# Performance work log

Hardware: AMD Instinct MI355X
Metric: run time of the kernel (lower is better)

The kernel has to match this reference:

```python
import jax, jax.numpy as jnp
import numpy as np

N_NODES = 50000
NUM_LAYERS = 3
D = 128
NUM_LABELS = 16
NUM_EDGES = 1600000


def setup_inputs() -> dict:
    key = jax.random.key(0)
    ks = jax.random.split(key, 6)
    s = 1.0 / np.sqrt(D)
    x = jax.random.normal(ks[0], (N_NODES, D), dtype=jnp.float32)
    edge_index = jax.random.randint(ks[1], (2, NUM_EDGES), 0, N_NODES, dtype=jnp.int64)
    W1 = jax.random.normal(ks[2], (NUM_LAYERS, D, D), dtype=jnp.float32) * s
    b1 = jnp.zeros((NUM_LAYERS, D), dtype=jnp.float32)
    W2 = jax.random.normal(ks[3], (NUM_LAYERS, D, D), dtype=jnp.float32) * s
    b2 = jnp.zeros((NUM_LAYERS, D), dtype=jnp.float32)
    Wc = jax.random.normal(ks[4], (D, NUM_LABELS), dtype=jnp.float32) * s
    bc = jnp.zeros((NUM_LABELS,), dtype=jnp.float32)
    return {"x": x, "edge_index": edge_index, "W1": W1, "b1": b1,
            "W2": W2, "b2": b2, "Wc": Wc, "bc": bc}


def reference(x, edge_index, W1, b1, W2, b2, Wc, bc):
    # PyG GINConv (default eps=0): h_i = MLP((1+eps)*x_i + sum_{j->i} x_j)
    src, dst = edge_index[0], edge_index[1]
    h = x
    for l in range(NUM_LAYERS):
        agg = jax.ops.segment_sum(h[src], dst, num_segments=N_NODES)  # [N, D]
        z = h + agg
        h = jax.nn.relu(z @ W1[l] + b1[l]) @ W2[l] + b2[l]
    logits = h @ Wc + bc
    return (h, logits)
```

## Files before the change

### kernel.cpp

```cpp
#include <hip/hip_runtime.h>

#define DD 128
#define CHUNK 6144
#define NBMAX 512
#define SCAP 8192
#define PADSLACK 2048

typedef __attribute__((ext_vector_type(8))) short bf16x8;
typedef __attribute__((ext_vector_type(4))) float f32x4;

__device__ __forceinline__ unsigned bf16rne(float f) {
  unsigned u = __float_as_uint(f);
  return (u + 0x7FFFu + ((u >> 16) & 1u)) >> 16;
}
__device__ __forceinline__ unsigned packbf(float lo, float hi) {
  return bf16rne(lo) | (bf16rne(hi) << 16);
}
__device__ __forceinline__ float bflo(unsigned v) { return __uint_as_float(v << 16); }
__device__ __forceinline__ float bfhi(unsigned v) { return __uint_as_float(v & 0xFFFF0000u); }

__device__ void block_scan_incl(int* cnt, int* inc, int nb, int tid) {
  for (int i = tid; i < nb; i += 256) inc[i] = cnt[i];
  __syncthreads();
  for (int d = 1; d < nb; d <<= 1) {
    int i0 = tid, i1 = tid + 256;
    int v0 = 0, v1 = 0;
    if (i0 < nb && i0 >= d) v0 = inc[i0 - d];
    if (i1 < nb && i1 >= d) v1 = inc[i1 - d];
    __syncthreads();
    if (i0 < nb) inc[i0] += v0;
    if (i1 < nb) inc[i1] += v1;
    __syncthreads();
  }
}

__global__ __launch_bounds__(256) void s1_hist(const int* __restrict__ dst,
                                               int* __restrict__ bucketCount, int e) {
  __shared__ int h[NBMAX];
  int tid = threadIdx.x;
  for (int i = tid; i < NBMAX; i += 256) h[i] = 0;
  __syncthreads();
  int i0 = blockIdx.x * CHUNK;
  int i1 = min(i0 + CHUNK, e);
  for (int i = i0 + tid; i < i1; i += 256) atomicAdd(&h[dst[i] >> 7], 1);
  __syncthreads();
  for (int i = tid; i < NBMAX; i += 256)
    if (h[i]) atomicAdd(&bucketCount[i], h[i]);
}

__global__ __launch_bounds__(256) void s2_scan(const int* __restrict__ bucketCount,
                                               int* __restrict__ bucketOff,
                                               int* __restrict__ gCursor,
                                               int* __restrict__ rs, int nb, int n, int e) {
  __shared__ int cnt[NBMAX], inc[NBMAX];
  int tid = threadIdx.x;
  for (int i = tid; i < nb; i += 256) cnt[i] = bucketCount[i];
  __syncthreads();
  block_scan_incl(cnt, inc, nb, tid);
  for (int i = tid; i < nb; i += 256) {
    int off = inc[i] - cnt[i];
    bucketOff[i] = off;
    gCursor[i] = off;
  }
  if (tid == 0) { bucketOff[nb] = e; rs[n] = e; }
}

__global__ __launch_bounds__(256) void s3_scatter(const int* __restrict__ src,
                                                  const int* __restrict__ dst,
                                                  int* __restrict__ gCursor,
                                                  unsigned int* __restrict__ bucketed,
                                                  int e, int nb) {
  __shared__ int cnt[NBMAX], inc[NBMAX], base[NBMAX], cur[NBMAX];
  __shared__ unsigned int pairs[CHUNK];
  int tid = threadIdx.x;
  for (int i = tid; i < nb; i += 256) cnt[i] = 0;
  __syncthreads();
  int i0 = blockIdx.x * CHUNK;
  int i1 = min(i0 + CHUNK, e);
  for (int i = i0 + tid; i < i1; i += 256) atomicAdd(&cnt[dst[i] >> 7], 1);
  __syncthreads();
  block_scan_incl(cnt, inc, nb, tid);
  for (int b = tid; b < nb; b += 256) {
    int c = cnt[b];
    base[b] = c ? atomicAdd(&gCursor[b], c) : 0;
    cur[b] = inc[b] - c;
  }
  __syncthreads();
  for (int i = i0 + tid; i < i1; i += 256) {
    int d = dst[i];
    int p = atomicAdd(&cur[d >> 7], 1);
    pairs[p] = (unsigned)d | ((unsigned)src[i] << 16);
  }
  __syncthreads();
  int m = i1 - i0;
  for (int i = tid; i < m; i += 256) {
    unsigned w = pairs[i];
    int b = (int)(w & 0xFFFFu) >> 7;
    bucketed[base[b] + (i - (inc[b] - cnt[b]))] = w;
  }
}

__global__ __launch_bounds__(256) void s4_fill(const unsigned int* __restrict__ bucketed,
                                               const int* __restrict__ bucketOff,
                                               int* __restrict__ rs,
                                               unsigned short* __restrict__ pdeg,
                                               unsigned short* __restrict__ ssrc, int n) {
  __shared__ int cnt[128], pin[128], cur[128];
  __shared__ unsigned short outb[SCAP];
  int b = blockIdx.x;
  int bo = bucketOff[b], b1 = bucketOff[b + 1];
  int len = b1 - bo;
  int pstart = bo + b * PADSLACK;
  int tid = threadIdx.x;
  int n0 = b << 7;
  if (tid < 128) cnt[tid] = 0;
  __syncthreads();
  for (int i = tid; i < len; i += 256) atomicAdd(&cnt[bucketed[bo + i] & 127], 1);
  __syncthreads();
  int pc = 0;
  if (tid < 128) {
    pc = max(16, (cnt[tid] + 15) & ~15);
    pin[tid] = pc;
  }
  __syncthreads();
  for (int d = 1; d < 128; d <<= 1) {
    int v = 0;
    if (tid < 128 && tid >= d) v = pin[tid - d];
    __syncthreads();
    if (tid < 128) pin[tid] += v;
    __syncthreads();
  }
  int plen = pin[127];
  if (tid < 128) {
    int off = pin[tid] - pc;
    cur[tid] = off;
    int node = n0 + tid;
    if (node < n) {
      rs[node] = pstart + off;
      pdeg[node] = (unsigned short)pc;
    }
  }
  __syncthreads();
  if (plen <= SCAP) {
    for (int i = tid; i < plen; i += 256) outb[i] = (unsigned short)n;
    __syncthreads();
    for (int i = tid; i < len; i += 256) {
      unsigned w = bucketed[bo + i];
      int p = atomicAdd(&cur[w & 127], 1);
      outb[p] = (unsigned short)(w >> 16);
    }
    __syncthreads();
    for (int i = tid; i < plen; i += 256) ssrc[pstart + i] = outb[i];
  } else {
    for (int i = tid; i < plen; i += 256) ssrc[pstart + i] = (unsigned short)n;
    __syncthreads();
    for (int i = tid; i < len; i += 256) {
      unsigned w = bucketed[bo + i];
      int p = atomicAdd(&cur[w & 127], 1);
      ssrc[pstart + p] = (unsigned short)(w >> 16);
    }
  }
}

__global__ __launch_bounds__(256) void conv_bf16(const float* __restrict__ x,
                                                 unsigned int* __restrict__ hb,
                                                 int n64, int total64) {
  int i = blockIdx.x * 256 + threadIdx.x;
  if (i < n64) {
    float2 v = ((const float2*)x)[i];
    hb[i] = packbf(v.x, v.y);
  } else if (i < total64) {
    hb[i] = 0u;
  }
}

__global__ __launch_bounds__(256) void prep_w(const float* __restrict__ W1,
                                              const float* __restrict__ W2,
                                              short* __restrict__ wt) {
  int idx = blockIdx.x * 256 + threadIdx.x;
  if (idx >= 3 * 2 * 16384) return;
  int lm = idx >> 14;
  int e = idx & 16383;
  int k = e >> 7;
  int col = e & 127;
  int layer = lm >> 1, mat = lm & 1;
  const float* W = mat ? W2 : W1;
  float w = W[layer * 16384 + k * 128 + col];
  unsigned short h = (unsigned short)bf16rne(w);
  int ksw = k ^ ((col & 7) << 3);
  wt[(size_t)lm * 16384 + col * 128 + ksw] = (short)h;
}

__global__ __launch_bounds__(256) void gather_zb(const unsigned int* __restrict__ hb,
                                                 const int* __restrict__ rs,
                                                 const unsigned short* __restrict__ pdeg,
                                                 const unsigned short* __restrict__ ssrc,
                                                 unsigned int* __restrict__ zb, int n) {
  int node = blockIdx.x * 4 + (threadIdx.x >> 6);
  if (node >= n) return;
  int lane = threadIdx.x & 63;
  int s0 = rs[node];
  int m = pdeg[node];
  unsigned v = hb[(unsigned)node * 64u + lane];
  float ax = bflo(v), ay = bfhi(v);
  unsigned A[16], B[16];
#pragma unroll
  for (int i = 0; i < 16; ++i)
    A[i] = hb[(unsigned)ssrc[s0 + i] * 64u + lane];
  int t1 = s0 + m;
  for (int t = s0 + 16; t < t1; t += 16) {
#pragma unroll
    for (int i = 0; i < 16; ++i)
      B[i] = hb[(unsigned)ssrc[t + i] * 64u + lane];
#pragma unroll
    for (int i = 0; i < 16; ++i) {
      ax += bflo(A[i]);
      ay += bfhi(A[i]);
    }
#pragma unroll
    for (int i = 0; i < 16; ++i) A[i] = B[i];
  }
#pragma unroll
  for (int i = 0; i < 16; ++i) {
    ax += bflo(A[i]);
    ay += bfhi(A[i]);
  }
  zb[(unsigned)node * 64u + lane] = packbf(ax, ay);
}

__global__ __launch_bounds__(256, 2) void mlp_mfma(
    const unsigned int* __restrict__ zb,
    const short* __restrict__ Wt1, const short* __restrict__ Wt2,
    const float* __restrict__ b1, const float* __restrict__ b2,
    float* __restrict__ fout, unsigned short* __restrict__ hbout,
    const float* __restrict__ Wc, const float* __restrict__ bc,
    float* __restrict__ lout, int n) {
  __shared__ char wbuf[32768];
  __shared__ char hsb[128 * 256];
  int tid = threadIdx.x;
  int w = tid >> 6, lane = tid & 63;
  int lr = lane & 15, hi = lane >> 4;
  int wr = (w & 1) * 64;
  int wc = (w >> 1) * 64;
  int node0 = blockIdx.x * 128;

  bf16x8 a[4][4];
#pragma unroll
  for (int t = 0; t < 4; ++t) {
    int row = node0 + wr + t * 16 + lr;
    row = min(row, n - 1);
    const char* rp = (const char*)(zb + (size_t)row * 64);
#pragma unroll
    for (int ks = 0; ks < 4; ++ks)
      a[t][ks] = *(const bf16x8*)(rp + ks * 64 + hi * 16);
  }

  f32x4 acc[4][4];
#pragma unroll
  for (int ct = 0; ct < 4; ++ct) {
    float bb = b1[wc + ct * 16 + lr];
#pragma unroll
    for (int t = 0; t < 4; ++t) acc[t][ct] = (f32x4){bb, bb, bb, bb};
  }

  {
    const char* gs = (const char*)Wt1;
    for (int i = tid * 16; i < 32768; i += 256 * 16)
      *(float4*)&wbuf[i] = *(const float4*)(gs + i);
  }
  __syncthreads();
#pragma unroll
  for (int ct = 0; ct < 4; ++ct) {
    int col = wc + ct * 16 + lr;
    int cx = (col & 7) << 4;
#pragma unroll
    for (int ks = 0; ks < 4; ++ks) {
      bf16x8 b = *(const bf16x8*)&wbuf[(col * 256 + ks * 64 + hi * 16) ^ cx];
#pragma unroll
      for (int t = 0; t < 4; ++t)
        acc[t][ct] = __builtin_amdgcn_mfma_f32_16x16x32_bf16(a[t][ks], b, acc[t][ct], 0, 0, 0);
    }
  }

#pragma unroll
  for (int t = 0; t < 4; ++t)
#pragma unroll
    for (int ct = 0; ct < 4; ++ct)
#pragma unroll
      for (int r = 0; r < 4; ++r) {
        int row = wr + t * 16 + hi * 4 + r;
        int col = wc + ct * 16 + lr;
        float v = fmaxf(acc[t][ct][r], 0.f);
        int byte = (row * 256 + col * 2) ^ ((row & 7) << 4);
        *(unsigned short*)&hsb[byte] = (unsigned short)bf16rne(v);
      }
  __syncthreads();

  bf16x8 a2[4][4];
#pragma unroll
  for (int t = 0; t < 4; ++t) {
    int row = wr + t * 16 + lr;
    int xr = (row & 7) << 4;
#pragma unroll
    for (int ks = 0; ks < 4; ++ks)
      a2[t][ks] = *(const bf16x8*)&hsb[(row * 256 + ks * 64 + hi * 16) ^ xr];
  }

#pragma unroll
  for (int ct = 0; ct < 4; ++ct) {
    float bb = b2[wc + ct * 16 + lr];
#pragma unroll
    for (int t = 0; t < 4; ++t) acc[t][ct] = (f32x4){bb, bb, bb, bb};
  }

  __syncthreads();
  {
    const char* gs = (const char*)Wt2;
    for (int i = tid * 16; i < 32768; i += 256 * 16)
      *(float4*)&wbuf[i] = *(const float4*)(gs + i);
  }
  __syncthreads();
#pragma unroll
  for (int ct = 0; ct < 4; ++ct) {
    int col = wc + ct * 16 + lr;
    int cx = (col & 7) << 4;
#pragma unroll
    for (int ks = 0; ks < 4; ++ks) {
      bf16x8 b = *(const bf16x8*)&wbuf[(col * 256 + ks * 64 + hi * 16) ^ cx];
#pragma unroll
      for (int t = 0; t < 4; ++t)
        acc[t][ct] = __builtin_amdgcn_mfma_f32_16x16x32_bf16(a2[t][ks], b, acc[t][ct], 0, 0, 0);
    }
  }

#pragma unroll
  for (int t = 0; t < 4; ++t)
#pragma unroll
    for (int ct = 0; ct < 4; ++ct)
#pragma unroll
      for (int r = 0; r < 4; ++r) {
        int node = node0 + wr + t * 16 + hi * 4 + r;
        if (node < n) {
          int col = wc + ct * 16 + lr;
          float v = acc[t][ct][r];
          if (fout) fout[(size_t)node * DD + col] = v;
          if (hbout) hbout[(size_t)node * DD + col] = (unsigned short)bf16rne(v);
        }
      }

  if (lout) {
    __syncthreads();
    float* wcb = (float*)wbuf;
    for (int i = tid; i < DD * 16; i += 256) wcb[i] = Wc[i];
#pragma unroll
    for (int t = 0; t < 4; ++t)
#pragma unroll
      for (int ct = 0; ct < 4; ++ct)
#pragma unroll
        for (int r = 0; r < 4; ++r) {
          int row = wr + t * 16 + hi * 4 + r;
          int col = wc + ct * 16 + lr;
          int byte = (row * 256 + col * 2) ^ ((row & 7) << 4);
          *(unsigned short*)&hsb[byte] = (unsigned short)bf16rne(acc[t][ct][r]);
        }
    __syncthreads();
    int node = tid >> 1;
    int lbase = (tid & 1) * 8;
    float lacc[8];
#pragma unroll
    for (int j = 0; j < 8; ++j) lacc[j] = bc[lbase + j];
    int xr = (node & 7) << 4;
    for (int c = 0; c < DD; ++c) {
      unsigned short hv16 = *(const unsigned short*)&hsb[(node * 256 + c * 2) ^ xr];
      float hv = __uint_as_float((unsigned)hv16 << 16);
      const float* wrow = &wcb[c * 16 + lbase];
#pragma unroll
      for (int j = 0; j < 8; ++j) lacc[j] += hv * wrow[j];
    }
    int gn = node0 + node;
    if (gn < n) {
#pragma unroll
      for (int j = 0; j < 8; ++j) lout[(size_t)gn * 16 + lbase + j] = lacc[j];
    }
  }
}

extern "C" void kernel_launch(void* const* d_in, const int* in_sizes, int n_in,
                              void* d_out, int out_size, void* d_ws, size_t ws_size,
                              hipStream_t stream) {
  const float* x = (const float*)d_in[0];
  const int* ei = (const int*)d_in[1];
  const float* W1 = (const float*)d_in[2];
  const float* b1 = (const float*)d_in[3];
  const float* W2 = (const float*)d_in[4];
  const float* b2 = (const float*)d_in[5];
  const float* Wc = (const float*)d_in[6];
  const float* bc = (const float*)d_in[7];

  const int N = in_sizes[0] / DD;
  const int E = in_sizes[1] / 2;
  const int* src = ei;
  const int* dst = ei + E;
  const int NB = (N + 127) >> 7;

  float* outp = (float*)d_out;
  float* h_final = outp;
  float* logits = outp + (size_t)N * DD;

  char* ws = (char*)d_ws;
  size_t off = 0;
  auto alloc = [&](size_t bytes) {
    char* p = ws + off;
    off = (off + bytes + 255) & ~(size_t)255;
    return p;
  };
  unsigned int* zb = (unsigned int*)alloc((size_t)N * 64 * 4);
  unsigned int* hb = (unsigned int*)alloc((size_t)(N + 1) * 64 * 4);
  short* wt = (short*)alloc((size_t)3 * 2 * 16384 * 2);
  int* bucketCount = (int*)alloc(NBMAX * 4);
  int* bucketOff = (int*)alloc((NBMAX + 1) * 4);
  int* gCursor = (int*)alloc(NBMAX * 4);
  int* rs = (int*)alloc((size_t)(N + 1) * 4);
  unsigned short* pdeg = (unsigned short*)alloc((size_t)N * 2);
  unsigned int* bucketed = (unsigned int*)alloc((size_t)E * 4);
  unsigned short* ssrc = (unsigned short*)alloc(((size_t)E + (size_t)NB * PADSLACK) * 2);

  const int gEdge = (E + CHUNK - 1) / CHUNK;
  const int gGather = (N + 3) / 4;
  const int gMlp = (N + 127) / 128;
  const int total64 = (N + 1) * 64;

  hipMemsetAsync(bucketCount, 0, NBMAX * 4, stream);
  s1_hist<<<gEdge, 256, 0, stream>>>(dst, bucketCount, E);
  s2_scan<<<1, 256, 0, stream>>>(bucketCount, bucketOff, gCursor, rs, NB, N, E);
  s3_scatter<<<gEdge, 256, 0, stream>>>(src, dst, gCursor, bucketed, E, NB);
  s4_fill<<<NB, 256, 0, stream>>>(bucketed, bucketOff, rs, pdeg, ssrc, N);

  prep_w<<<(3 * 2 * 16384 + 255) / 256, 256, 0, stream>>>(W1, W2, wt);
  conv_bf16<<<(total64 + 255) / 256, 256, 0, stream>>>(x, hb, N * 64, total64);

  auto WT = [&](int layer, int mat) { return wt + ((size_t)(layer * 2 + mat)) * 16384; };

  gather_zb<<<gGather, 256, 0, stream>>>(hb, rs, pdeg, ssrc, zb, N);
  mlp_mfma<<<gMlp, 256, 0, stream>>>(zb, WT(0, 0), WT(0, 1), b1, b2,
                                     nullptr, (unsigned short*)hb, nullptr, nullptr, nullptr, N);
  gather_zb<<<gGather, 256, 0, stream>>>(hb, rs, pdeg, ssrc, zb, N);
  mlp_mfma<<<gMlp, 256, 0, stream>>>(zb, WT(1, 0), WT(1, 1), b1 + DD, b2 + DD,
                                     nullptr, (unsigned short*)hb, nullptr, nullptr, nullptr, N);
  gather_zb<<<gGather, 256, 0, stream>>>(hb, rs, pdeg, ssrc, zb, N);
  mlp_mfma<<<gMlp, 256, 0, stream>>>(zb, WT(2, 0), WT(2, 1), b1 + 2 * DD, b2 + 2 * DD,
                                     h_final, nullptr, Wc, bc, logits, N);
}
```

Baseline: 273.9 us.

## Fuse setup kernels, pad neighbor lists to 8, dual-node gather, MFMA classifier

Merges the histogram, bf16 conversion and weight-prep kernels into one launch, and also preps a swizzled bf16 copy of the classifier weights. Neighbor-list padding drops from multiples of 16 to 8 to cut wasted gather loads, and each wavefront now gathers two nodes with interleaved 8-wide batches to expose more memory parallelism. The mlp kernel prefetches W2 into registers before the first GEMM's epilogue to drop a barrier, and computes logits with MFMA instead of a scalar loop. These changes add register pressure in the gather and mlp kernels and reduce per-node load batching depth.

```diff
diff --git a/kernel.cpp b/kernel.cpp
--- a/kernel.cpp
+++ b/kernel.cpp
@@ -4,7 +4,7 @@
 #define CHUNK 6144
 #define NBMAX 512
 #define SCAP 8192
-#define PADSLACK 2048
+#define PADSLACK 1024
 
 typedef __attribute__((ext_vector_type(8))) short bf16x8;
 typedef __attribute__((ext_vector_type(4))) float f32x4;
@@ -34,18 +34,53 @@
   }
 }
 
-__global__ __launch_bounds__(256) void s1_hist(const int* __restrict__ dst,
-                                               int* __restrict__ bucketCount, int e) {
-  __shared__ int h[NBMAX];
+__global__ __launch_bounds__(256) void setup_fat(
+    const int* __restrict__ dst, int* __restrict__ bucketCount, int e,
+    const float* __restrict__ x, unsigned int* __restrict__ hb, int n64, int total64,
+    const float* __restrict__ W1, const float* __restrict__ W2,
+    const float* __restrict__ Wc, short* __restrict__ wt,
+    int nS1, int nConv) {
+  int b = blockIdx.x;
   int tid = threadIdx.x;
-  for (int i = tid; i < NBMAX; i += 256) h[i] = 0;
-  __syncthreads();
-  int i0 = blockIdx.x * CHUNK;
-  int i1 = min(i0 + CHUNK, e);
-  for (int i = i0 + tid; i < i1; i += 256) atomicAdd(&h[dst[i] >> 7], 1);
-  __syncthreads();
-  for (int i = tid; i < NBMAX; i += 256)
-    if (h[i]) atomicAdd(&bucketCount[i], h[i]);
+  if (b < nS1) {
+    __shared__ int h[NBMAX];
+    for (int i = tid; i < NBMAX; i += 256) h[i] = 0;
+    __syncthreads();
+    int i0 = b * CHUNK;
+    int i1 = min(i0 + CHUNK, e);
+    for (int i = i0 + tid; i < i1; i += 256) atomicAdd(&h[dst[i] >> 7], 1);
+    __syncthreads();
+    for (int i = tid; i < NBMAX; i += 256)
+      if (h[i]) atomicAdd(&bucketCount[i], h[i]);
+  } else if (b < nS1 + nConv) {
+    int i = (b - nS1) * 256 + tid;
+    if (i < n64) {
+      float2 v = ((const float2*)x)[i];
+      hb[i] = packbf(v.x, v.y);
+    } else if (i < total64) {
+      hb[i] = 0u;
+    }
+  } else {
+    int idx = (b - nS1 - nConv) * 256 + tid;
+    if (idx < 3 * 2 * 16384) {
+      int lm = idx >> 14;
+      int e2 = idx & 16383;
+      int k = e2 >> 7;
+      int col = e2 & 127;
+      int layer = lm >> 1, mat = lm & 1;
+      const float* W = mat ? W2 : W1;
+      float w = W[layer * 16384 + k * 128 + col];
+      int ksw = k ^ ((col & 7) << 3);
+      wt[(size_t)lm * 16384 + col * 128 + ksw] = (short)bf16rne(w);
+    } else if (idx < 3 * 2 * 16384 + 2048) {
+      int e2 = idx - 3 * 2 * 16384;
+      int k = e2 >> 4;
+      int col = e2 & 15;
+      float w = Wc[k * 16 + col];
+      int ksw = k ^ ((col & 7) << 3);
+      wt[(size_t)6 * 16384 + col * 128 + ksw] = (short)bf16rne(w);
+    }
+  }
 }
 
 __global__ __launch_bounds__(256) void s2_scan(const int* __restrict__ bucketCount,
@@ -119,7 +154,7 @@
   __syncthreads();
   int pc = 0;
   if (tid < 128) {
-    pc = max(16, (cnt[tid] + 15) & ~15);
+    pc = max(8, (cnt[tid] + 7) & ~7);
     pin[tid] = pc;
   }
   __syncthreads();
@@ -162,70 +197,83 @@
   }
 }
 
-__global__ __launch_bounds__(256) void conv_bf16(const float* __restrict__ x,
-                                                 unsigned int* __restrict__ hb,
-                                                 int n64, int total64) {
-  int i = blockIdx.x * 256 + threadIdx.x;
-  if (i < n64) {
-    float2 v = ((const float2*)x)[i];
-    hb[i] = packbf(v.x, v.y);
-  } else if (i < total64) {
-    hb[i] = 0u;
-  }
-}
-
-__global__ __launch_bounds__(256) void prep_w(const float* __restrict__ W1,
-                                              const float* __restrict__ W2,
-                                              short* __restrict__ wt) {
-  int idx = blockIdx.x * 256 + threadIdx.x;
-  if (idx >= 3 * 2 * 16384) return;
-  int lm = idx >> 14;
-  int e = idx & 16383;
-  int k = e >> 7;
-  int col = e & 127;
-  int layer = lm >> 1, mat = lm & 1;
-  const float* W = mat ? W2 : W1;
-  float w = W[layer * 16384 + k * 128 + col];
-  unsigned short h = (unsigned short)bf16rne(w);
-  int ksw = k ^ ((col & 7) << 3);
-  wt[(size_t)lm * 16384 + col * 128 + ksw] = (short)h;
-}
-
 __global__ __launch_bounds__(256) void gather_zb(const unsigned int* __restrict__ hb,
                                                  const int* __restrict__ rs,
                                                  const unsigned short* __restrict__ pdeg,
                                                  const unsigned short* __restrict__ ssrc,
                                                  unsigned int* __restrict__ zb, int n) {
-  int node = blockIdx.x * 4 + (threadIdx.x >> 6);
-  if (node >= n) return;
+  int pair = blockIdx.x * 4 + (threadIdx.x >> 6);
+  int nA = pair * 2;
+  if (nA >= n) return;
+  int nB = nA + 1;
+  bool hasB = nB < n;
   int lane = threadIdx.x & 63;
-  int s0 = rs[node];
-  int m = pdeg[node];
-  unsigned v = hb[(unsigned)node * 64u + lane];
-  float ax = bflo(v), ay = bfhi(v);
-  unsigned A[16], B[16];
-#pragma unroll
-  for (int i = 0; i < 16; ++i)
-    A[i] = hb[(unsigned)ssrc[s0 + i] * 64u + lane];
-  int t1 = s0 + m;
-  for (int t = s0 + 16; t < t1; t += 16) {
-#pragma unroll
-    for (int i = 0; i < 16; ++i)
-      B[i] = hb[(unsigned)ssrc[t + i] * 64u + lane];
-#pragma unroll
-    for (int i = 0; i < 16; ++i) {
-      ax += bflo(A[i]);
-      ay += bfhi(A[i]);
-    }
-#pragma unroll
-    for (int i = 0; i < 16; ++i) A[i] = B[i];
-  }
-#pragma unroll
-  for (int i = 0; i < 16; ++i) {
-    ax += bflo(A[i]);
-    ay += bfhi(A[i]);
-  }
-  zb[(unsigned)node * 64u + lane] = packbf(ax, ay);
+  int sA = rs[nA], mA = pdeg[nA];
+  int sB = hasB ? rs[nB] : sA;
+  int mB = hasB ? pdeg[nB] : 0;
+
+  unsigned vA = hb[(unsigned)nA * 64u + lane];
+  float ax0 = bflo(vA), ay0 = bfhi(vA);
+  float ax1 = 0.f, ay1 = 0.f;
+  if (hasB) {
+    unsigned vB = hb[(unsigned)nB * 64u + lane];
+    ax1 = bflo(vB); ay1 = bfhi(vB);
+  }
+
+  unsigned A0[8], B0[8], A1[8], B1[8];
+#pragma unroll
+  for (int i = 0; i < 8; ++i) A0[i] = hb[(unsigned)ssrc[sA + i] * 64u + lane];
+  if (hasB) {
+#pragma unroll
+    for (int i = 0; i < 8; ++i) A1[i] = hb[(unsigned)ssrc[sB + i] * 64u + lane];
+  }
+  int iA = sA + 8, eA = sA + mA;
+  int iB = sB + 8, eB = sB + mB;
+
+  if (hasB) {
+    while (iA < eA && iB < eB) {
+#pragma unroll
+      for (int i = 0; i < 8; ++i) B0[i] = hb[(unsigned)ssrc[iA + i] * 64u + lane];
+#pragma unroll
+      for (int i = 0; i < 8; ++i) B1[i] = hb[(unsigned)ssrc[iB + i] * 64u + lane];
+#pragma unroll
+      for (int i = 0; i < 8; ++i) {
+        ax0 += bflo(A0[i]); ay0 += bfhi(A0[i]); A0[i] = B0[i];
+      }
+#pragma unroll
+      for (int i = 0; i < 8; ++i) {
+        ax1 += bflo(A1[i]); ay1 += bfhi(A1[i]); A1[i] = B1[i];
+      }
+      iA += 8; iB += 8;
+    }
+  }
+  while (iA < eA) {
+#pragma unroll
+    for (int i = 0; i < 8; ++i) B0[i] = hb[(unsigned)ssrc[iA + i] * 64u + lane];
+#pragma unroll
+    for (int i = 0; i < 8; ++i) {
+      ax0 += bflo(A0[i]); ay0 += bfhi(A0[i]); A0[i] = B0[i];
+    }
+    iA += 8;
+  }
+#pragma unroll
+  for (int i = 0; i < 8; ++i) { ax0 += bflo(A0[i]); ay0 += bfhi(A0[i]); }
+  zb[(unsigned)nA * 64u + lane] = packbf(ax0, ay0);
+
+  if (hasB) {
+    while (iB < eB) {
+#pragma unroll
+      for (int i = 0; i < 8; ++i) B1[i] = hb[(unsigned)ssrc[iB + i] * 64u + lane];
+#pragma unroll
+      for (int i = 0; i < 8; ++i) {
+        ax1 += bflo(A1[i]); ay1 += bfhi(A1[i]); A1[i] = B1[i];
+      }
+      iB += 8;
+    }
+#pragma unroll
+    for (int i = 0; i < 8; ++i) { ax1 += bflo(A1[i]); ay1 += bfhi(A1[i]); }
+    zb[(unsigned)nB * 64u + lane] = packbf(ax1, ay1);
+  }
 }
 
 __global__ __launch_bounds__(256, 2) void mlp_mfma(
@@ -233,7 +281,7 @@
     const short* __restrict__ Wt1, const short* __restrict__ Wt2,
     const float* __restrict__ b1, const float* __restrict__ b2,
     float* __restrict__ fout, unsigned short* __restrict__ hbout,
-    const float* __restrict__ Wc, const float* __restrict__ bc,
+    const short* __restrict__ WcI, const float* __restrict__ bc,
     float* __restrict__ lout, int n) {
   __shared__ char wbuf[32768];
   __shared__ char hsb[128 * 256];
@@ -282,6 +330,11 @@
     }
   }
 
+  float4 w2r[8];
+#pragma unroll
+  for (int i = 0; i < 8; ++i)
+    w2r[i] = *(const float4*)((const char*)Wt2 + tid * 16 + i * 4096);
+
 #pragma unroll
   for (int t = 0; t < 4; ++t)
 #pragma unroll
@@ -305,6 +358,9 @@
     for (int ks = 0; ks < 4; ++ks)
       a2[t][ks] = *(const bf16x8*)&hsb[(row * 256 + ks * 64 + hi * 16) ^ xr];
   }
+#pragma unroll
+  for (int i = 0; i < 8; ++i)
+    *(float4*)&wbuf[tid * 16 + i * 4096] = w2r[i];
 
 #pragma unroll
   for (int ct = 0; ct < 4; ++ct) {
@@ -312,14 +368,8 @@
 #pragma unroll
     for (int t = 0; t < 4; ++t) acc[t][ct] = (f32x4){bb, bb, bb, bb};
   }
-
-  __syncthreads();
-  {
-    const char* gs = (const char*)Wt2;
-    for (int i = tid * 16; i < 32768; i += 256 * 16)
-      *(float4*)&wbuf[i] = *(const float4*)(gs + i);
-  }
-  __syncthreads();
+  __syncthreads();
+
 #pragma unroll
   for (int ct = 0; ct < 4; ++ct) {
     int col = wc + ct * 16 + lr;
@@ -349,9 +399,6 @@
       }
 
   if (lout) {
-    __syncthreads();
-    float* wcb = (float*)wbuf;
-    for (int i = tid; i < DD * 16; i += 256) wcb[i] = Wc[i];
 #pragma unroll
     for (int t = 0; t < 4; ++t)
 #pragma unroll
@@ -364,24 +411,37 @@
           *(unsigned short*)&hsb[byte] = (unsigned short)bf16rne(acc[t][ct][r]);
         }
     __syncthreads();
-    int node = tid >> 1;
-    int lbase = (tid & 1) * 8;
-    float lacc[8];
-#pragma unroll
-    for (int j = 0; j < 8; ++j) lacc[j] = bc[lbase + j];
-    int xr = (node & 7) << 4;
-    for (int c = 0; c < DD; ++c) {
-      unsigned short hv16 = *(const unsigned short*)&hsb[(node * 256 + c * 2) ^ xr];
-      float hv = __uint_as_float((unsigned)hv16 << 16);
-      const float* wrow = &wcb[c * 16 + lbase];
-#pragma unroll
-      for (int j = 0; j < 8; ++j) lacc[j] += hv * wrow[j];
-    }
-    int gn = node0 + node;
-    if (gn < n) {
-#pragma unroll
-      for (int j = 0; j < 8; ++j) lout[(size_t)gn * 16 + lbase + j] = lacc[j];
-    }
+    bf16x8 a3[4][4];
+#pragma unroll
+    for (int t = 0; t < 4; ++t) {
+      int row = wr + t * 16 + lr;
+      int xr = (row & 7) << 4;
+#pragma unroll
+      for (int ks = 0; ks < 4; ++ks)
+        a3[t][ks] = *(const bf16x8*)&hsb[(row * 256 + ks * 64 + hi * 16) ^ xr];
+    }
+    const char* wci = (const char*)WcI;
+    bf16x8 bw[4];
+    int cxc = (lr & 7) << 4;
+#pragma unroll
+    for (int ks = 0; ks < 4; ++ks)
+      bw[ks] = *(const bf16x8*)&wci[(lr * 256 + ks * 64 + hi * 16) ^ cxc];
+    f32x4 acc3[4];
+    float bb = bc[lr];
+#pragma unroll
+    for (int t = 0; t < 4; ++t) acc3[t] = (f32x4){bb, bb, bb, bb};
+#pragma unroll
+    for (int t = 0; t < 4; ++t)
+#pragma unroll
+      for (int ks = 0; ks < 4; ++ks)
+        acc3[t] = __builtin_amdgcn_mfma_f32_16x16x32_bf16(a3[t][ks], bw[ks], acc3[t], 0, 0, 0);
+#pragma unroll
+    for (int t = 0; t < 4; ++t)
+#pragma unroll
+      for (int r = 0; r < 4; ++r) {
+        int gn = node0 + wr + t * 16 + hi * 4 + r;
+        if (gn < n) lout[(size_t)gn * 16 + lr] = acc3[t][r];
+      }
   }
 }
 
@@ -416,7 +476,7 @@
   };
   unsigned int* zb = (unsigned int*)alloc((size_t)N * 64 * 4);
   unsigned int* hb = (unsigned int*)alloc((size_t)(N + 1) * 64 * 4);
-  short* wt = (short*)alloc((size_t)3 * 2 * 16384 * 2);
+  short* wt = (short*)alloc((size_t)(3 * 2 * 16384 + 2048) * 2);
   int* bucketCount = (int*)alloc(NBMAX * 4);
   int* bucketOff = (int*)alloc((NBMAX + 1) * 4);
   int* gCursor = (int*)alloc(NBMAX * 4);
@@ -426,20 +486,21 @@
   unsigned short* ssrc = (unsigned short*)alloc(((size_t)E + (size_t)NB * PADSLACK) * 2);
 
   const int gEdge = (E + CHUNK - 1) / CHUNK;
-  const int gGather = (N + 3) / 4;
+  const int gGather = ((N + 1) / 2 + 3) / 4;
   const int gMlp = (N + 127) / 128;
   const int total64 = (N + 1) * 64;
+  const int nConv = (total64 + 255) / 256;
+  const int nPrep = (3 * 2 * 16384 + 2048 + 255) / 256;
 
   hipMemsetAsync(bucketCount, 0, NBMAX * 4, stream);
-  s1_hist<<<gEdge, 256, 0, stream>>>(dst, bucketCount, E);
+  setup_fat<<<gEdge + nConv + nPrep, 256, 0, stream>>>(
+      dst, bucketCount, E, x, hb, N * 64, total64, W1, W2, Wc, wt, gEdge, nConv);
   s2_scan<<<1, 256, 0, stream>>>(bucketCount, bucketOff, gCursor, rs, NB, N, E);
   s3_scatter<<<gEdge, 256, 0, stream>>>(src, dst, gCursor, bucketed, E, NB);
   s4_fill<<<NB, 256, 0, stream>>>(bucketed, bucketOff, rs, pdeg, ssrc, N);
 
-  prep_w<<<(3 * 2 * 16384 + 255) / 256, 256, 0, stream>>>(W1, W2, wt);
-  conv_bf16<<<(total64 + 255) / 256, 256, 0, stream>>>(x, hb, N * 64, total64);
-
   auto WT = [&](int layer, int mat) { return wt + ((size_t)(layer * 2 + mat)) * 16384; };
+  const short* WcI = wt + (size_t)6 * 16384;
 
   gather_zb<<<gGather, 256, 0, stream>>>(hb, rs, pdeg, ssrc, zb, N);
   mlp_mfma<<<gMlp, 256, 0, stream>>>(zb, WT(0, 0), WT(0, 1), b1, b2,
@@ -449,5 +510,5 @@
                                      nullptr, (unsigned short*)hb, nullptr, nullptr, nullptr, N);
   gather_zb<<<gGather, 256, 0, stream>>>(hb, rs, pdeg, ssrc, zb, N);
   mlp_mfma<<<gMlp, 256, 0, stream>>>(zb, WT(2, 0), WT(2, 1), b1 + 2 * DD, b2 + 2 * DD,
-                                     h_final, nullptr, Wc, bc, logits, N);
-}
+                                     h_final, nullptr, WcI, bc, logits, N);
+}
```

Measured after the change: 263.0 us. 1.04x faster.
